# Performance work log

Hardware: AMD Instinct MI355X
Metric: run time of the kernel (lower is better)

Reference implementation:

```python
import jax, jax.numpy as jnp
import numpy as np

B, T, C = 2, 2048, 1024
H, D = 16, 64  # n_head, head_size = C // H


def setup_inputs() -> dict:
    key = jax.random.key(0)
    ks = jax.random.split(key, 6)
    s = 1.0 / np.sqrt(C)
    x = jax.random.normal(ks[0], (B, T, C), dtype=jnp.float32)
    Wq = jax.random.normal(ks[1], (C, C), dtype=jnp.float32) * s
    Wk = jax.random.normal(ks[2], (C, C), dtype=jnp.float32) * s
    Wv = jax.random.normal(ks[3], (C, C), dtype=jnp.float32) * s
    Wp = jax.random.normal(ks[4], (C, C), dtype=jnp.float32) * s
    bp = jnp.zeros((C,), dtype=jnp.float32)
    return {"x": x, "Wq": Wq, "Wk": Wk, "Wv": Wv, "Wp": Wp, "bp": bp}


def _feature_map(x):
    # F.elu(x) + 1.0
    return jnp.where(x > 0, x + 1.0, jnp.exp(x))


def reference(x, Wq, Wk, Wv, Wp, bp):
    Bx, Tx, Cx = x.shape
    # q,k,v projections (nn.Linear with weight W applies x @ W.T)
    q = (x @ Wq.T).reshape(Bx, Tx, H, D).transpose(0, 2, 1, 3)  # bhtd
    k = (x @ Wk.T).reshape(Bx, Tx, H, D).transpose(0, 2, 1, 3)
    v = (x @ Wv.T).reshape(Bx, Tx, H, D).transpose(0, 2, 1, 3)
    qp = _feature_map(q)
    kp = _feature_map(k)
    # cumulative outer-product context: (B,H,T,D,D)
    kv_cum = jnp.cumsum(jnp.einsum('bhsd,bhsv->bhsdv', kp, v), axis=2)
    ksum_cum = jnp.cumsum(kp, axis=2)  # (B,H,T,D)
    num = jnp.einsum('bhsd,bhsdv->bhsv', qp, kv_cum)
    den = jnp.einsum('bhsd,bhsd->bhs', qp, ksum_cum)[..., None] + 1e-6
    y = (num / den).transpose(0, 2, 1, 3).reshape(Bx, Tx, Cx)
    out = y @ Wp.T + bp  # dropout(p=0) is identity
    new_kv = kv_cum[:, :, -1]
    new_ksum = ksum_cum[:, :, -1]
    return (out, new_kv, new_ksum)
```

## Files before the change

kernel.cpp:

```cpp
#include <hip/hip_runtime.h>
#include <math.h>

#define BB 2
#define TT 2048
#define CC 1024
#define HH 16
#define DD 64
#define MM (BB*TT)
#define LCH 128
#define NCH (TT/LCH)
#define BHH (BB*HH)

#define OUT_OFF_KV   4194304
#define OUT_OFF_KSUM 4325376
#define MB 1048576

typedef unsigned int u32;
typedef unsigned short u16;
typedef __attribute__((ext_vector_type(8))) short s16x8;
typedef __attribute__((ext_vector_type(8))) unsigned short us8;
typedef __attribute__((ext_vector_type(4))) float f32x4;

__device__ __forceinline__ float fmap(float x) {
    return x > 0.0f ? x + 1.0f : expf(x);
}
__device__ __forceinline__ u16 bf16r(float f) {
    u32 u = __float_as_uint(f);
    u += 0x7fffu + ((u >> 16) & 1u);
    return (u16)(u >> 16);
}
__device__ __forceinline__ float bf2f(u16 u) {
    return __uint_as_float(((u32)u) << 16);
}
__device__ __forceinline__ void gload16(const void* g, void* l) {
    __builtin_amdgcn_global_load_lds(
        (const __attribute__((address_space(1))) u32*)g,
        (__attribute__((address_space(3))) u32*)l, 16, 0, 0);
}

__global__ __launch_bounds__(256)
void f2bf_all(const float* __restrict__ x,
              const float* __restrict__ Wq, const float* __restrict__ Wk,
              const float* __restrict__ Wv, const float* __restrict__ Wp,
              u16* __restrict__ xbf, u16* __restrict__ wbf)
{
    const int i = blockIdx.x * 256 + threadIdx.x;
    const float* src;
    u16* dst;
    int off;
    if (i < 524288) {
        src = x; dst = xbf; off = i;
    } else {
        const int j = i - 524288;
        const int sel = j >> 17;
        off = j & 131071;
        src = (sel == 0) ? Wq : (sel == 1) ? Wk : (sel == 2) ? Wv : Wp;
        dst = wbf + ((size_t)sel << 20);
    }
    const float4 a = ((const float4*)src)[off*2];
    const float4 b = ((const float4*)src)[off*2 + 1];
    us8 p;
    p[0]=bf16r(a.x); p[1]=bf16r(a.y); p[2]=bf16r(a.z); p[3]=bf16r(a.w);
    p[4]=bf16r(b.x); p[5]=bf16r(b.y); p[6]=bf16r(b.z); p[7]=bf16r(b.w);
    ((us8*)dst)[off] = p;
}

__device__ __forceinline__ void read_a(const char* LB, int abase, int wm, int lr, int lg4,
                                       s16x8 (&af)[4][2])
{
    #pragma unroll
    for (int mi = 0; mi < 4; ++mi) {
        const int r = wm*64 + mi*16 + lr;
        #pragma unroll
        for (int ks = 0; ks < 2; ++ks) {
            const int gg = (ks*4 + lg4) ^ (r & 7);
            af[mi][ks] = *(const s16x8*)(LB + abase + r*128 + gg*16);
        }
    }
}
__device__ __forceinline__ void read_b(const char* LB, int bbase, int wn, int lr, int lg4,
                                       s16x8 (&bv)[2][2])
{
    #pragma unroll
    for (int ni = 0; ni < 2; ++ni) {
        const int r = wn*32 + ni*16 + lr;
        #pragma unroll
        for (int ks = 0; ks < 2; ++ks) {
            const int gg = (ks*4 + lg4) ^ (r & 7);
            bv[ni][ks] = *(const s16x8*)(LB + bbase + r*128 + gg*16);
        }
    }
}
__device__ __forceinline__ void phase_mfma(const s16x8 (&af)[4][2], const s16x8 (&bv)[2][2],
                                           f32x4 (&acc)[4][2])
{
    #pragma unroll
    for (int mi = 0; mi < 4; ++mi)
        #pragma unroll
        for (int ni = 0; ni < 2; ++ni)
            #pragma unroll
            for (int ks = 0; ks < 2; ++ks)
                acc[mi][ni] = __builtin_amdgcn_mfma_f32_16x16x32_bf16(
                    af[mi][ks], bv[ni][ks], acc[mi][ni], 0, 0, 0);
}

__global__ __launch_bounds__(512, 2)
void lca_gemm_qkv8(const u16* __restrict__ A, const u16* __restrict__ Wall,
                   u16* __restrict__ qp, u16* __restrict__ kp,
                   u16* __restrict__ kt, u16* __restrict__ vt)
{
    extern __shared__ char LB[];
    const int tid  = threadIdx.x;
    const int lane = tid & 63;
    const int wid  = tid >> 6;
    const int wm   = wid >> 2;
    const int wn   = wid & 3;
    const int bm0  = blockIdx.y * 256;
    const int bn0g = blockIdx.x * 256;
    const int sel  = bn0g >> 10;
    const int nn0  = bn0g & (CC-1);
    const u16* W = Wall + ((size_t)sel << 20);
    const int NT = CC / 64;

    const int srow = (wid << 3) + (lane >> 3);
    const int sg   = lane & 7;
    auto STAGE = [&](const u16* G, int ldsbase) {
        #pragma unroll
        for (int j = 0; j < 2; ++j) {
            const int r  = j*64 + srow;
            const int gs = sg ^ (r & 7);
            gload16(G + (size_t)r * CC + gs*8,
                    LB + ldsbase + (size_t)(j*64 + (wid<<3))*128);
        }
    };
    #define LDSA(slot,h) (((slot)*2 + (h))*16384)
    #define LDSB(slot,h) (65536 + ((slot)*2 + (h))*16384)

    f32x4 acc[4][4][2];
    #pragma unroll
    for (int q = 0; q < 4; ++q)
        #pragma unroll
        for (int mi = 0; mi < 4; ++mi)
            #pragma unroll
            for (int ni = 0; ni < 2; ++ni)
                acc[q][mi][ni] = (f32x4){0.f, 0.f, 0.f, 0.f};

    STAGE(A + (size_t)(bm0      ) * CC + 0,  LDSA(0,0));
    STAGE(A + (size_t)(bm0 + 128) * CC + 0,  LDSA(0,1));
    STAGE(W + (size_t)(nn0      ) * CC + 0,  LDSB(0,0));
    STAGE(W + (size_t)(nn0 + 128) * CC + 0,  LDSB(0,1));
    STAGE(A + (size_t)(bm0      ) * CC + 64, LDSA(1,0));
    STAGE(W + (size_t)(nn0      ) * CC + 64, LDSB(1,0));
    asm volatile("s_waitcnt vmcnt(4)" ::: "memory");
    __builtin_amdgcn_s_barrier();

    const int lr  = lane & 15;
    const int lg4 = lane >> 4;

    s16x8 afr0[4][2], afr1[4][2], b0r[2][2], b1r[2][2];
    read_a(LB, LDSA(0,0), wm, lr, lg4, afr0);
    read_b(LB, LDSB(0,0), wn, lr, lg4, b0r);

    for (int t = 0; t < NT; ++t) {
        const int slot  = t & 1;
        const int nslot = slot ^ 1;

        if (t+1 < NT) STAGE(A + (size_t)(bm0 + 128)*CC + (t+1)*64, LDSA(nslot,1));
        read_b(LB, LDSB(slot,1), wn, lr, lg4, b1r);
        __builtin_amdgcn_sched_barrier(0);
        if (t < NT-1) asm volatile("s_waitcnt vmcnt(6)" ::: "memory");
        asm volatile("s_waitcnt lgkmcnt(4)" ::: "memory");
        __builtin_amdgcn_sched_barrier(0);
        __builtin_amdgcn_s_setprio(1);
        phase_mfma(afr0, b0r, acc[0]);
        __builtin_amdgcn_s_setprio(0);
        __builtin_amdgcn_sched_barrier(0);
        __builtin_amdgcn_s_barrier();

        if (t+1 < NT) STAGE(W + (size_t)(nn0 + 128)*CC + (t+1)*64, LDSB(nslot,1));
        read_a(LB, LDSA(slot,1), wm, lr, lg4, afr1);
        __builtin_amdgcn_sched_barrier(0);
        if (t < NT-1) asm volatile("s_waitcnt vmcnt(6)" ::: "memory");
        asm volatile("s_waitcnt lgkmcnt(8)" ::: "memory");
        __builtin_amdgcn_sched_barrier(0);
        __builtin_amdgcn_s_setprio(1);
        phase_mfma(afr0, b1r, acc[1]);
        __builtin_amdgcn_s_setprio(0);
        __builtin_amdgcn_sched_barrier(0);
        __builtin_amdgcn_s_barrier();

        if (t+2 < NT) STAGE(A + (size_t)(bm0)*CC + (t+2)*64, LDSA(slot,0));
        __builtin_amdgcn_sched_barrier(0);
        if (t < NT-1) asm volatile("s_waitcnt vmcnt(4)" ::: "memory");
        asm volatile("s_waitcnt lgkmcnt(0)" ::: "memory");
        __builtin_amdgcn_sched_barrier(0);
        __builtin_amdgcn_s_setprio(1);
        phase_mfma(afr1, b0r, acc[2]);
        __builtin_amdgcn_s_setprio(0);
        __builtin_amdgcn_sched_barrier(0);
        __builtin_amdgcn_s_barrier();

        if (t+2 < NT) STAGE(W + (size_t)(nn0)*CC + (t+2)*64, LDSB(slot,0));
        if (t+1 < NT) {
            read_a(LB, LDSA(nslot,0), wm, lr, lg4, afr0);
            read_b(LB, LDSB(nslot,0), wn, lr, lg4, b0r);
        }
        __builtin_amdgcn_sched_barrier(0);
        if (t < NT-2)       asm volatile("s_waitcnt vmcnt(4)" ::: "memory");
        else if (t == NT-2) asm volatile("s_waitcnt vmcnt(0)" ::: "memory");
        __builtin_amdgcn_sched_barrier(0);
        __builtin_amdgcn_s_setprio(1);
        phase_mfma(afr1, b1r, acc[3]);
        __builtin_amdgcn_s_setprio(0);
        __builtin_amdgcn_sched_barrier(0);
        __builtin_amdgcn_s_barrier();
    }

    #pragma unroll
    for (int q = 0; q < 4; ++q) {
        const int mh = q >> 1, nh = q & 1;
        #pragma unroll
        for (int mi = 0; mi < 4; ++mi) {
            #pragma unroll
            for (int ni = 0; ni < 2; ++ni) {
                const int coln = nn0 + nh*128 + wn*32 + ni*16 + lr;
                const int rb   = bm0 + mh*128 + wm*64 + mi*16 + lg4*4;
                const int h = coln >> 6, d = coln & (DD-1);
                const int b = rb >> 11, t0 = rb & (TT-1);
                u16 bvv[4];
                #pragma unroll
                for (int r = 0; r < 4; ++r) {
                    float val = acc[q][mi][ni][r];
                    if (sel != 2) val = fmap(val);
                    bvv[r] = bf16r(val);
                }
                if (sel == 0) {
                    u16* p = qp + (((size_t)(b*HH + h)) * TT + t0) * DD + d;
                    #pragma unroll
                    for (int r = 0; r < 4; ++r) p[(size_t)r * DD] = bvv[r];
                } else {
                    const int ch = t0 >> 7, tc = t0 & (LCH-1);
                    u16* pt = (sel == 1 ? kt : vt)
                            + (((size_t)((b*HH + h)*NCH + ch)) * DD + d) * LCH + tc;
                    *(ushort4*)pt = make_ushort4(bvv[0], bvv[1], bvv[2], bvv[3]);
                    if (sel == 1) {
                        u16* p = kp + (((size_t)(b*HH + h)) * TT + t0) * DD + d;
                        #pragma unroll
                        for (int r = 0; r < 4; ++r) p[(size_t)r * DD] = bvv[r];
                    }
                }
            }
        }
    }
    #undef LDSA
    #undef LDSB
}

__global__ __launch_bounds__(256)
void lca_gemm_out(const u16* __restrict__ A, const u16* __restrict__ W,
                  const float* __restrict__ bias, float* __restrict__ out)
{
    __shared__ short As[2][4096];
    __shared__ short Bs2[2][2048];
    const int tid  = threadIdx.x;
    const int lane = tid & 63;
    const int wid  = tid >> 6;
    const int bm0 = blockIdx.y * 128;
    const int bn0 = blockIdx.x * 64;
    const int wm = wid >> 1, wn = wid & 1;

    const int rsA = wid*32 + (lane >> 2);
    const int rsB = wid*16 + (lane >> 2);
    const int kc  = (lane & 3) * 8;

    f32x4 acc[4][2];
    #pragma unroll
    for (int i = 0; i < 4; ++i)
        #pragma unroll
        for (int j = 0; j < 2; ++j)
            acc[i][j] = (f32x4){0.f, 0.f, 0.f, 0.f};

    const int rA = wm*64 + (lane & 15);
    const int rB = wn*32 + (lane & 15);
    const int kk = (lane >> 4) * 8;

    #pragma unroll
    for (int j = 0; j < 2; ++j)
        gload16(A + (size_t)(bm0 + rsA + j*16) * CC + kc, &As[0][wid*1024 + j*512]);
    gload16(W + (size_t)(bn0 + rsB) * CC + kc, &Bs2[0][wid*512]);
    __syncthreads();

    int cur = 0;
    for (int k0 = 0; k0 < CC; k0 += 32) {
        if (k0 + 32 < CC) {
            #pragma unroll
            for (int j = 0; j < 2; ++j)
                gload16(A + (size_t)(bm0 + rsA + j*16) * CC + k0 + 32 + kc, &As[cur^1][wid*1024 + j*512]);
            gload16(W + (size_t)(bn0 + rsB) * CC + k0 + 32 + kc, &Bs2[cur^1][wid*512]);
        }

        s16x8 af[4], bf[2];
        #pragma unroll
        for (int mi = 0; mi < 4; ++mi) af[mi] = *(const s16x8*)(&As[cur][(rA + mi*16)*32 + kk]);
        #pragma unroll
        for (int ni = 0; ni < 2; ++ni) bf[ni] = *(const s16x8*)(&Bs2[cur][(rB + ni*16)*32 + kk]);
        #pragma unroll
        for (int mi = 0; mi < 4; ++mi)
            #pragma unroll
            for (int ni = 0; ni < 2; ++ni)
                acc[mi][ni] = __builtin_amdgcn_mfma_f32_16x16x32_bf16(af[mi], bf[ni], acc[mi][ni], 0, 0, 0);

        __syncthreads();
        cur ^= 1;
    }

    #pragma unroll
    for (int mi = 0; mi < 4; ++mi) {
        #pragma unroll
        for (int ni = 0; ni < 2; ++ni) {
            const int col = bn0 + wn*32 + ni*16 + (lane & 15);
            const int rb  = bm0 + wm*64 + mi*16 + (lane >> 4)*4;
            const float bb = bias[col];
            #pragma unroll
            for (int r = 0; r < 4; ++r)
                out[(size_t)(rb + r) * CC + col] = acc[mi][ni][r] + bb;
        }
    }
}

__global__ __launch_bounds__(256)
void lca_pass1(const u16* __restrict__ kt, const u16* __restrict__ vt,
               float* __restrict__ Sloc, float* __restrict__ ksloc)
{
    const int wid = threadIdx.x >> 6, lane = threadIdx.x & 63;
    const int c = blockIdx.x * 4 + wid, bh = blockIdx.y;
    const u16* kg = kt + ((size_t)bh * NCH + c) * DD * LCH;
    const u16* vg = vt + ((size_t)bh * NCH + c) * DD * LCH;
    const int lr = lane & 15;
    const int lk = (lane >> 4) * 8;

    f32x4 acc[4][4];
    #pragma unroll
    for (int i = 0; i < 4; ++i)
        #pragma unroll
        for (int j = 0; j < 4; ++j)
            acc[i][j] = (f32x4){0.f, 0.f, 0.f, 0.f};

    #pragma unroll
    for (int ks = 0; ks < 4; ++ks) {
        const int k = ks*32 + lk;
        s16x8 af[4], bf[4];
        #pragma unroll
        for (int mi = 0; mi < 4; ++mi) af[mi] = *(const s16x8*)(kg + (size_t)(mi*16 + lr)*LCH + k);
        #pragma unroll
        for (int ni = 0; ni < 4; ++ni) bf[ni] = *(const s16x8*)(vg + (size_t)(ni*16 + lr)*LCH + k);
        #pragma unroll
        for (int mi = 0; mi < 4; ++mi)
            #pragma unroll
            for (int ni = 0; ni < 4; ++ni)
                acc[mi][ni] = __builtin_amdgcn_mfma_f32_16x16x32_bf16(af[mi], bf[ni], acc[mi][ni], 0, 0, 0);
    }

    float* So = Sloc + ((size_t)bh * NCH + c) * (DD*DD);
    #pragma unroll
    for (int mi = 0; mi < 4; ++mi)
        #pragma unroll
        for (int ni = 0; ni < 4; ++ni) {
            const int e = ni*16 + lr;
            #pragma unroll
            for (int r = 0; r < 4; ++r) {
                const int d = mi*16 + (lane >> 4)*4 + r;
                So[(size_t)d * DD + e] = acc[mi][ni][r];
            }
        }

    float s = 0.0f;
    #pragma unroll
    for (int i = 0; i < 16; ++i) {
        s16x8 dv = *(const s16x8*)(kg + (size_t)lane * LCH + i*8);
        #pragma unroll
        for (int j = 0; j < 8; ++j) s += bf2f((u16)dv[j]);
    }
    ksloc[((size_t)bh * NCH + c) * DD + lane] = s;
}

__global__ __launch_bounds__(256)
void lca_pass2(const float* __restrict__ Sloc, const float* __restrict__ ksloc,
               u16* __restrict__ pst, float* __restrict__ pksx,
               float* __restrict__ out)
{
    const int bh = blockIdx.x;
    const int tid = threadIdx.x;
    const int d0 = (tid >> 4) * 4;
    const int e0 = (tid & 15) * 4;

    float run[4][4] = {};
    for (int c = 0; c < NCH; ++c) {
        u16* P = pst + ((size_t)bh * NCH + c) * (DD*DD);
        #pragma unroll
        for (int i = 0; i < 4; ++i)
            #pragma unroll
            for (int j = 0; j < 4; ++j)
                P[(size_t)(e0 + j) * DD + (d0 + i)] = bf16r(run[i][j]);
        const float* S = Sloc + ((size_t)bh * NCH + c) * (DD*DD);
        #pragma unroll
        for (int i = 0; i < 4; ++i) {
            const float4 t4 = *(const float4*)(S + (size_t)(d0 + i) * DD + e0);
            run[i][0] += t4.x; run[i][1] += t4.y; run[i][2] += t4.z; run[i][3] += t4.w;
        }
    }
    float* nkv = out + OUT_OFF_KV + (size_t)bh * (DD*DD);
    #pragma unroll
    for (int i = 0; i < 4; ++i)
        *(float4*)(nkv + (size_t)(d0 + i) * DD + e0) =
            make_float4(run[i][0], run[i][1], run[i][2], run[i][3]);

    if (tid < DD) {
        float r = 0.0f;
        for (int c = 0; c < NCH; ++c) {
            pksx[((size_t)bh * NCH + c) * DD + tid] = r;
            r += ksloc[((size_t)bh * NCH + c) * DD + tid];
        }
        out[OUT_OFF_KSUM + (size_t)bh * DD + tid] = r;
    }
}

__global__ __launch_bounds__(256)
void lca_pass3(const u16* __restrict__ qp, const u16* __restrict__ kp,
               const u16* __restrict__ vt, const u16* __restrict__ pst,
               const float* __restrict__ pksx, u16* __restrict__ ybf)
{
    __shared__ short SA[16384];
    __shared__ short VS[8192];
    __shared__ short PS[4096];
    __shared__ float pks_s[DD];
    __shared__ float den_s[LCH];

    char* SAb = (char*)SA;
    char* VSb = (char*)VS;
    char* PSb = (char*)PS;

    const int c = blockIdx.x, bh = blockIdx.y;
    const int tid = threadIdx.x;
    const int lane = tid & 63, wid = tid >> 6;

    const u16* qg = qp + ((size_t)bh * TT + (size_t)c * LCH) * DD;
    const u16* kg = kp + ((size_t)bh * TT + (size_t)c * LCH) * DD;
    const u16* vg = vt + ((size_t)bh * NCH + c) * DD * LCH;
    const u16* pg = pst + ((size_t)bh * NCH + c) * (DD*DD);

    for (int i = tid; i < 1024; i += 256) {
        const int row = i >> 3, cc = i & 7;
        const s16x8 dv = *(const s16x8*)(qg + (size_t)row*DD + cc*8);
        *(s16x8*)(SAb + ((row*128 + cc*16) ^ ((row & 7) << 4))) = dv;
    }
    for (int i = tid; i < 1024; i += 256) {
        const int row = i >> 3, cc = i & 7;
        const s16x8 dv = *(const s16x8*)(kg + (size_t)row*DD + cc*8);
        *(s16x8*)(SAb + 16384 + ((row*128 + cc*16) ^ ((row & 7) << 4))) = dv;
    }
    for (int i = tid; i < 1024; i += 256) {
        const int row = i >> 4, cc = i & 15;
        const s16x8 dv = *(const s16x8*)(vg + (size_t)row*LCH + cc*8);
        *(s16x8*)(VSb + ((row*256 + cc*16) ^ ((row & 7) << 4))) = dv;
    }
    for (int i = tid; i < 512; i += 256) {
        const int row = i >> 3, cc = i & 7;
        const s16x8 dv = *(const s16x8*)(pg + (size_t)row*DD + cc*8);
        *(s16x8*)(PSb + ((row*128 + cc*16) ^ ((row & 7) << 4))) = dv;
    }
    if (tid < DD) pks_s[tid] = pksx[((size_t)bh * NCH + c) * DD + tid];
    __syncthreads();

    if (tid < LCH) {
        const int t = tid;
        float s = 1e-6f;
        #pragma unroll
        for (int cc = 0; cc < 8; ++cc) {
            const s16x8 dv = *(const s16x8*)(SAb + ((t*128 + cc*16) ^ ((t & 7) << 4)));
            #pragma unroll
            for (int j = 0; j < 8; ++j) s += bf2f((u16)dv[j]) * pks_s[cc*8 + j];
        }
        den_s[t] = s;
    }

    const int wrow0 = wid * 32;
    const int lr = lane & 15;
    const int lg = lane >> 4;
    const int lk = lg * 8;

    f32x4 sacc[2][8];
    #pragma unroll
    for (int mi = 0; mi < 2; ++mi)
        #pragma unroll
        for (int ni = 0; ni < 8; ++ni)
            sacc[mi][ni] = (f32x4){0.f, 0.f, 0.f, 0.f};

    #pragma unroll
    for (int ks = 0; ks < 2; ++ks) {
        const int k2 = (ks*32 + lk) * 2;
        s16x8 af[2];
        #pragma unroll
        for (int mi = 0; mi < 2; ++mi) {
            const int row = wrow0 + mi*16 + lr;
            af[mi] = *(const s16x8*)(SAb + ((row*128 + k2) ^ ((row & 7) << 4)));
        }
        #pragma unroll
        for (int ni = 0; ni < 8; ++ni) {
            const int rowb = ni*16 + lr;
            const s16x8 bf = *(const s16x8*)(SAb + 16384 + ((rowb*128 + k2) ^ ((rowb & 7) << 4)));
            sacc[0][ni] = __builtin_amdgcn_mfma_f32_16x16x32_bf16(af[0], bf, sacc[0][ni], 0, 0, 0);
            sacc[1][ni] = __builtin_amdgcn_mfma_f32_16x16x32_bf16(af[1], bf, sacc[1][ni], 0, 0, 0);
        }
    }

    f32x4 pv[2][4];
    #pragma unroll
    for (int mi = 0; mi < 2; ++mi)
        #pragma unroll
        for (int ni = 0; ni < 4; ++ni)
            pv[mi][ni] = (f32x4){0.f, 0.f, 0.f, 0.f};

    #pragma unroll
    for (int ks = 0; ks < 2; ++ks) {
        const int k2 = (ks*32 + lk) * 2;
        s16x8 af[2];
        #pragma unroll
        for (int mi = 0; mi < 2; ++mi) {
            const int row = wrow0 + mi*16 + lr;
            af[mi] = *(const s16x8*)(SAb + ((row*128 + k2) ^ ((row & 7) << 4)));
        }
        #pragma unroll
        for (int ni = 0; ni < 4; ++ni) {
            const int rowb = ni*16 + lr;
            const s16x8 bf = *(const s16x8*)(PSb + ((rowb*128 + k2) ^ ((rowb & 7) << 4)));
            pv[0][ni] = __builtin_amdgcn_mfma_f32_16x16x32_bf16(af[0], bf, pv[0][ni], 0, 0, 0);
            pv[1][ni] = __builtin_amdgcn_mfma_f32_16x16x32_bf16(af[1], bf, pv[1][ni], 0, 0, 0);
        }
    }
    __syncthreads();

    #pragma unroll
    for (int mi = 0; mi < 2; ++mi) {
        float dr[4] = {0.f, 0.f, 0.f, 0.f};
        #pragma unroll
        for (int ni = 0; ni < 8; ++ni) {
            const int tp = ni*16 + lr;
            #pragma unroll
            for (int r = 0; r < 4; ++r) {
                const int t = wrow0 + mi*16 + lg*4 + r;
                const float v = (tp <= t) ? sacc[mi][ni][r] : 0.f;
                dr[r] += v;
                *(u16*)(SAb + ((t*256 + tp*2) ^ ((t & 7) << 4))) = bf16r(v);
            }
        }
        #pragma unroll
        for (int r = 0; r < 4; ++r) {
            float s = dr[r];
            s += __shfl_xor(s, 1); s += __shfl_xor(s, 2);
            s += __shfl_xor(s, 4); s += __shfl_xor(s, 8);
            if (lr == 0) {
                const int t = wrow0 + mi*16 + lg*4 + r;
                den_s[t] += s;
            }
        }
    }
    __syncthreads();

    #pragma unroll
    for (int ks = 0; ks < 4; ++ks) {
        const int k2 = (ks*32 + lk) * 2;
        s16x8 af[2];
        #pragma unroll
        for (int mi = 0; mi < 2; ++mi) {
            const int row = wrow0 + mi*16 + lr;
            af[mi] = *(const s16x8*)(SAb + ((row*256 + k2) ^ ((row & 7) << 4)));
        }
        #pragma unroll
        for (int ni = 0; ni < 4; ++ni) {
            const int rowb = ni*16 + lr;
            const s16x8 bf = *(const s16x8*)(VSb + ((rowb*256 + k2) ^ ((rowb & 7) << 4)));
            pv[0][ni] = __builtin_amdgcn_mfma_f32_16x16x32_bf16(af[0], bf, pv[0][ni], 0, 0, 0);
            pv[1][ni] = __builtin_amdgcn_mfma_f32_16x16x32_bf16(af[1], bf, pv[1][ni], 0, 0, 0);
        }
    }

    const int b = bh >> 4, h = bh & (HH-1);
    #pragma unroll
    for (int mi = 0; mi < 2; ++mi)
        #pragma unroll
        for (int ni = 0; ni < 4; ++ni) {
            const int e = ni*16 + lr;
            #pragma unroll
            for (int r = 0; r < 4; ++r) {
                const int t = wrow0 + mi*16 + lg*4 + r;
                const float y = pv[mi][ni][r] / den_s[t];
                ybf[((size_t)(b*TT) + (size_t)c*LCH + t) * CC + h*DD + e] = bf16r(y);
            }
        }
}

extern "C" void kernel_launch(void* const* d_in, const int* in_sizes, int n_in,
                              void* d_out, int out_size, void* d_ws, size_t ws_size,
                              hipStream_t stream) {
    const float* x  = (const float*)d_in[0];
    const float* Wq = (const float*)d_in[1];
    const float* Wk = (const float*)d_in[2];
    const float* Wv = (const float*)d_in[3];
    const float* Wp = (const float*)d_in[4];
    const float* bp = (const float*)d_in[5];
    float* out = (float*)d_out;
    char* ws = (char*)d_ws;

    u16*   xbf  = (u16*)(ws + 0);
    u16*   Wbf  = (u16*)(ws + (size_t)8*MB);
    u16*   qp   = (u16*)(ws + (size_t)16*MB);
    u16*   kp   = (u16*)(ws + (size_t)24*MB);
    u16*   kt   = (u16*)(ws + (size_t)32*MB);
    u16*   vt   = (u16*)(ws + (size_t)40*MB);
    u16*   ybf  = (u16*)(ws + (size_t)48*MB);
    float* Sl   = (float*)(ws + (size_t)56*MB);
    float* ksl  = (float*)(ws + (size_t)64*MB);
    float* pksx = (float*)(ws + (size_t)64*MB + 131072);
    u16*   pst  = (u16*)(ws + (size_t)65*MB);

    (void)hipFuncSetAttribute((const void*)lca_gemm_qkv8,
                              hipFuncAttributeMaxDynamicSharedMemorySize, 131072);

    f2bf_all<<<4096, 256, 0, stream>>>(x, Wq, Wk, Wv, Wp, xbf, Wbf);

    lca_gemm_qkv8<<<dim3(3*CC/256, MM/256), 512, 131072, stream>>>(xbf, Wbf, qp, kp, kt, vt);

    lca_pass1<<<dim3(NCH/4, BHH), 256, 0, stream>>>(kt, vt, Sl, ksl);
    lca_pass2<<<BHH, 256, 0, stream>>>(Sl, ksl, pst, pksx, out);
    lca_pass3<<<dim3(NCH, BHH), 256, 0, stream>>>(qp, kp, vt, pst, pksx, ybf);

    lca_gemm_out<<<dim3(CC/64, MM/128), 256, 0, stream>>>(ybf, Wbf + ((size_t)3 << 20), bp, out);
}
```

Before: 124.8 us.

## Fuse chunk-state and prefix-scan passes into one kernel; swizzle output GEMM blocks

```diff
diff --git a/kernel.cpp b/kernel.cpp
--- a/kernel.cpp
+++ b/kernel.cpp
@@ -265,8 +265,12 @@
     const int tid  = threadIdx.x;
     const int lane = tid & 63;
     const int wid  = tid >> 6;
-    const int bm0 = blockIdx.y * 128;
-    const int bn0 = blockIdx.x * 64;
+
+    const int bid = blockIdx.y * gridDim.x + blockIdx.x;
+    const int nb  = (bid & 7) * 64 + (bid >> 3);
+    const int bm0 = (nb >> 4) * 128;
+    const int bn0 = (nb & 15) * 64;
+
     const int wm = wid >> 1, wn = wid & 1;
 
     const int rsA = wid*32 + (lane >> 2);
@@ -328,27 +332,18 @@
     }
 }
 
-__global__ __launch_bounds__(256)
-void lca_pass1(const u16* __restrict__ kt, const u16* __restrict__ vt,
-               float* __restrict__ Sloc, float* __restrict__ ksloc)
-{
-    const int wid = threadIdx.x >> 6, lane = threadIdx.x & 63;
-    const int c = blockIdx.x * 4 + wid, bh = blockIdx.y;
-    const u16* kg = kt + ((size_t)bh * NCH + c) * DD * LCH;
-    const u16* vg = vt + ((size_t)bh * NCH + c) * DD * LCH;
-    const int lr = lane & 15;
-    const int lk = (lane >> 4) * 8;
-
-    f32x4 acc[4][4];
-    #pragma unroll
-    for (int i = 0; i < 4; ++i)
-        #pragma unroll
-        for (int j = 0; j < 4; ++j)
-            acc[i][j] = (f32x4){0.f, 0.f, 0.f, 0.f};
-
-    #pragma unroll
-    for (int ks = 0; ks < 4; ++ks) {
-        const int k = ks*32 + lk;
+__device__ __forceinline__ void chunk_S(const u16* __restrict__ kg, const u16* __restrict__ vg,
+                                        int lr, int lk, int lane,
+                                        f32x4 (&acc)[4][4], float& ks)
+{
+    #pragma unroll
+    for (int mi = 0; mi < 4; ++mi)
+        #pragma unroll
+        for (int ni = 0; ni < 4; ++ni)
+            acc[mi][ni] = (f32x4){0.f, 0.f, 0.f, 0.f};
+    #pragma unroll
+    for (int kss = 0; kss < 4; ++kss) {
+        const int k = kss*32 + lk;
         s16x8 af[4], bf[4];
         #pragma unroll
         for (int mi = 0; mi < 4; ++mi) af[mi] = *(const s16x8*)(kg + (size_t)(mi*16 + lr)*LCH + k);
@@ -360,68 +355,108 @@
             for (int ni = 0; ni < 4; ++ni)
                 acc[mi][ni] = __builtin_amdgcn_mfma_f32_16x16x32_bf16(af[mi], bf[ni], acc[mi][ni], 0, 0, 0);
     }
-
-    float* So = Sloc + ((size_t)bh * NCH + c) * (DD*DD);
-    #pragma unroll
-    for (int mi = 0; mi < 4; ++mi)
-        #pragma unroll
-        for (int ni = 0; ni < 4; ++ni) {
-            const int e = ni*16 + lr;
-            #pragma unroll
-            for (int r = 0; r < 4; ++r) {
-                const int d = mi*16 + (lane >> 4)*4 + r;
-                So[(size_t)d * DD + e] = acc[mi][ni][r];
-            }
-        }
-
-    float s = 0.0f;
+    ks = 0.0f;
     #pragma unroll
     for (int i = 0; i < 16; ++i) {
         s16x8 dv = *(const s16x8*)(kg + (size_t)lane * LCH + i*8);
         #pragma unroll
-        for (int j = 0; j < 8; ++j) s += bf2f((u16)dv[j]);
-    }
-    ksloc[((size_t)bh * NCH + c) * DD + lane] = s;
-}
-
-__global__ __launch_bounds__(256)
-void lca_pass2(const float* __restrict__ Sloc, const float* __restrict__ ksloc,
-               u16* __restrict__ pst, float* __restrict__ pksx,
-               float* __restrict__ out)
-{
-    const int bh = blockIdx.x;
+        for (int j = 0; j < 8; ++j) ks += bf2f((u16)dv[j]);
+    }
+}
+
+__global__ __launch_bounds__(512, 2)
+void lca_pass12(const u16* __restrict__ kt, const u16* __restrict__ vt,
+                u16* __restrict__ pst, float* __restrict__ pksx,
+                float* __restrict__ out)
+{
+    extern __shared__ char P12[];
+    float* Tw  = (float*)P12;
+    float* ksw = (float*)(P12 + 131072);
+
+    const int bh  = blockIdx.x;
     const int tid = threadIdx.x;
-    const int d0 = (tid >> 4) * 4;
-    const int e0 = (tid & 15) * 4;
-
-    float run[4][4] = {};
-    for (int c = 0; c < NCH; ++c) {
-        u16* P = pst + ((size_t)bh * NCH + c) * (DD*DD);
-        #pragma unroll
-        for (int i = 0; i < 4; ++i)
-            #pragma unroll
-            for (int j = 0; j < 4; ++j)
-                P[(size_t)(e0 + j) * DD + (d0 + i)] = bf16r(run[i][j]);
-        const float* S = Sloc + ((size_t)bh * NCH + c) * (DD*DD);
-        #pragma unroll
-        for (int i = 0; i < 4; ++i) {
-            const float4 t4 = *(const float4*)(S + (size_t)(d0 + i) * DD + e0);
-            run[i][0] += t4.x; run[i][1] += t4.y; run[i][2] += t4.z; run[i][3] += t4.w;
-        }
-    }
-    float* nkv = out + OUT_OFF_KV + (size_t)bh * (DD*DD);
-    #pragma unroll
-    for (int i = 0; i < 4; ++i)
-        *(float4*)(nkv + (size_t)(d0 + i) * DD + e0) =
-            make_float4(run[i][0], run[i][1], run[i][2], run[i][3]);
-
-    if (tid < DD) {
-        float r = 0.0f;
-        for (int c = 0; c < NCH; ++c) {
-            pksx[((size_t)bh * NCH + c) * DD + tid] = r;
-            r += ksloc[((size_t)bh * NCH + c) * DD + tid];
-        }
-        out[OUT_OFF_KSUM + (size_t)bh * DD + tid] = r;
+    const int wid = tid >> 6, lane = tid & 63;
+    const int lr = lane & 15, lg = lane >> 4;
+    const int lk = lg * 8;
+    const int c0 = wid * 2;
+
+    const u16* kg0 = kt + ((size_t)bh * NCH + c0) * DD * LCH;
+    const u16* vg0 = vt + ((size_t)bh * NCH + c0) * DD * LCH;
+
+    f32x4 s0[4][4], s1[4][4];
+    float ks0, ks1;
+    chunk_S(kg0,              vg0,              lr, lk, lane, s0, ks0);
+    chunk_S(kg0 + DD*LCH,     vg0 + DD*LCH,     lr, lk, lane, s1, ks1);
+
+    float* Tme = Tw + wid * 4096;
+    #pragma unroll
+    for (int mi = 0; mi < 4; ++mi)
+        #pragma unroll
+        for (int ni = 0; ni < 4; ++ni)
+            #pragma unroll
+            for (int r = 0; r < 4; ++r) {
+                const int d = mi*16 + lg*4 + r;
+                const int e = ni*16 + lr;
+                Tme[d*64 + e] = s0[mi][ni][r] + s1[mi][ni][r];
+            }
+    ksw[wid*64 + lane] = ks0 + ks1;
+    __syncthreads();
+
+    f32x4 off[4][4];
+    #pragma unroll
+    for (int mi = 0; mi < 4; ++mi)
+        #pragma unroll
+        for (int ni = 0; ni < 4; ++ni)
+            off[mi][ni] = (f32x4){0.f, 0.f, 0.f, 0.f};
+    for (int w = 0; w < 8; ++w) {
+        if (w >= wid) break;
+        const float* Tp = Tw + w * 4096;
+        #pragma unroll
+        for (int mi = 0; mi < 4; ++mi)
+            #pragma unroll
+            for (int ni = 0; ni < 4; ++ni)
+                #pragma unroll
+                for (int r = 0; r < 4; ++r) {
+                    const int d = mi*16 + lg*4 + r;
+                    const int e = ni*16 + lr;
+                    off[mi][ni][r] += Tp[d*64 + e];
+                }
+    }
+    float koff = 0.0f;
+    for (int w = 0; w < 8; ++w) {
+        if (w >= wid) break;
+        koff += ksw[w*64 + lane];
+    }
+
+    u16* P0 = pst + ((size_t)bh * NCH + c0) * (DD*DD);
+    u16* P1 = P0 + DD*DD;
+    #pragma unroll
+    for (int mi = 0; mi < 4; ++mi)
+        #pragma unroll
+        for (int ni = 0; ni < 4; ++ni)
+            #pragma unroll
+            for (int r = 0; r < 4; ++r) {
+                const int d = mi*16 + lg*4 + r;
+                const int e = ni*16 + lr;
+                P0[(size_t)e * DD + d] = bf16r(off[mi][ni][r]);
+                P1[(size_t)e * DD + d] = bf16r(off[mi][ni][r] + s0[mi][ni][r]);
+            }
+    pksx[((size_t)bh * NCH + c0) * DD + lane]     = koff;
+    pksx[((size_t)bh * NCH + c0 + 1) * DD + lane] = koff + ks0;
+
+    if (wid == 7) {
+        float* nkv = out + OUT_OFF_KV + (size_t)bh * (DD*DD);
+        #pragma unroll
+        for (int mi = 0; mi < 4; ++mi)
+            #pragma unroll
+            for (int ni = 0; ni < 4; ++ni)
+                #pragma unroll
+                for (int r = 0; r < 4; ++r) {
+                    const int d = mi*16 + lg*4 + r;
+                    const int e = ni*16 + lr;
+                    nkv[(size_t)d * DD + e] = off[mi][ni][r] + s0[mi][ni][r] + s1[mi][ni][r];
+                }
+        out[OUT_OFF_KSUM + (size_t)bh * DD + lane] = koff + ks0 + ks1;
     }
 }
 
@@ -619,20 +654,19 @@
     u16*   kt   = (u16*)(ws + (size_t)32*MB);
     u16*   vt   = (u16*)(ws + (size_t)40*MB);
     u16*   ybf  = (u16*)(ws + (size_t)48*MB);
-    float* Sl   = (float*)(ws + (size_t)56*MB);
-    float* ksl  = (float*)(ws + (size_t)64*MB);
     float* pksx = (float*)(ws + (size_t)64*MB + 131072);
     u16*   pst  = (u16*)(ws + (size_t)65*MB);
 
     (void)hipFuncSetAttribute((const void*)lca_gemm_qkv8,
                               hipFuncAttributeMaxDynamicSharedMemorySize, 131072);
+    (void)hipFuncSetAttribute((const void*)lca_pass12,
+                              hipFuncAttributeMaxDynamicSharedMemorySize, 133120);
 
     f2bf_all<<<4096, 256, 0, stream>>>(x, Wq, Wk, Wv, Wp, xbf, Wbf);
 
     lca_gemm_qkv8<<<dim3(3*CC/256, MM/256), 512, 131072, stream>>>(xbf, Wbf, qp, kp, kt, vt);
 
-    lca_pass1<<<dim3(NCH/4, BHH), 256, 0, stream>>>(kt, vt, Sl, ksl);
-    lca_pass2<<<BHH, 256, 0, stream>>>(Sl, ksl, pst, pksx, out);
+    lca_pass12<<<BHH, 512, 133120, stream>>>(kt, vt, pst, pksx, out);
     lca_pass3<<<dim3(NCH, BHH), 256, 0, stream>>>(qp, kp, vt, pst, pksx, ybf);
 
     lca_gemm_out<<<dim3(CC/64, MM/128), 256, 0, stream>>>(ybf, Wbf + ((size_t)3 << 20), bp, out);
```

Result: slower. 180.9 us (+45.0%).
